# Kernel optimization log

Measured on AMD Instinct MI355X. Metric: run time of the kernel, lower is better.

The kernel has to match this reference:

```python
import jax, jax.numpy as jnp
import numpy as np

# Static hyperparams matching init_kwargs
KSIZE, STRIDE, PAD, DIL = 3, 2, 1, 1


def setup_inputs() -> dict:
    key = jax.random.key(0)
    k1, k2 = jax.random.split(key)
    B, H, W, Cin, Cout = 8, 128, 128, 128, 256
    feats = jax.random.normal(k1, (B * H * W, Cin), dtype=jnp.float32)
    weight = jax.random.normal(k2, (KSIZE * KSIZE, Cin, Cout), dtype=jnp.float32) * 0.05
    alpha_upper = jnp.ones((1,), dtype=jnp.float32)
    # dense grid coords [N, 3] = (batch, y, x), matching a dense image sparse tensor
    bb, yy, xx = np.meshgrid(np.arange(B), np.arange(H), np.arange(W), indexing='ij')
    coords = jnp.asarray(np.stack([bb, yy, xx], -1).reshape(-1, 3), dtype=jnp.int32)
    return {"feats": feats, "weight": weight, "alpha_upper": alpha_upper,
            "coords": coords, "H": H, "W": W, "B": B}


def _coord_ranges(H, W):
    # Faithful translation of WrappedMinkowskiStridedOperation.__init__ + forward
    # coordinate math, specialized to a dense grid (per-batch min=0, max=H-1/W-1).
    kernel_origin = DIL * ((KSIZE - 1) // 2) * (KSIZE % 2)
    dilated = DIL * (KSIZE - 1) + 1
    ks_off = kernel_origin - dilated + 1          # _kernel_start_offset
    ke_off = kernel_origin                        # _kernel_end_offset
    idx_start = kernel_origin - PAD               # _index_start_offset
    ranges = []
    for ext in (H, W):
        idx_end = (ext - 1) + kernel_origin + PAD - dilated + 2
        start = max(idx_start, (0 + ks_off - idx_start) // STRIDE * STRIDE + idx_start)
        end = min(idx_end, ((ext - 1 + ke_off - idx_start) // STRIDE + 1) * STRIDE + idx_start)
        ranges.append(np.arange(start, end, STRIDE))
    offsets = np.arange(KSIZE) * DIL - kernel_origin  # kernel region offsets
    return ranges[0], ranges[1], offsets, idx_start


def reference(feats, weight, alpha_upper, coords, H, W, B):
    Cin = feats.shape[1]
    Cout = weight.shape[-1]
    ys, xs, offs, idx_start = _coord_ranges(H, W)
    OH, OW = len(ys), len(xs)
    oy, ox = jnp.meshgrid(jnp.asarray(ys, jnp.int32), jnp.asarray(xs, jnp.int32), indexing='ij')
    dy, dx = np.meshgrid(offs, offs, indexing='ij')
    dy = jnp.asarray(dy.reshape(-1), jnp.int32)  # [kvol]
    dx = jnp.asarray(dx.reshape(-1), jnp.int32)
    ny = oy[None] + dy[:, None, None]            # [kvol, OH, OW]
    nx = ox[None] + dx[:, None, None]
    valid = (ny >= 0) & (ny < H) & (nx >= 0) & (nx < W)
    lin = jnp.clip(ny, 0, H - 1) * W + jnp.clip(nx, 0, W - 1)  # [kvol, OH, OW]
    feats3 = feats.reshape(B, H * W, Cin)
    gathered = feats3[:, lin]                    # [B, kvol, OH, OW, Cin]
    gathered = jnp.where(valid[None, ..., None], gathered, jnp.zeros((), feats.dtype))
    out = jnp.einsum('bkhwc,kcd->bhwd', gathered, weight)  # [B, OH, OW, Cout]
    out_feats = out.reshape(B * OH * OW, Cout)
    # output coordinates, remapped as in forward (shift by index_start, divide by stride)
    oc = jnp.stack([oy, ox], -1).reshape(-1, 2)  # [OH*OW, 2]
    oc = (oc - jnp.int32(idx_start)) // jnp.int32(STRIDE)
    oc = jnp.tile(oc, (B, 1))
    bcol = jnp.repeat(jnp.arange(B, dtype=jnp.int32), OH * OW)
    out_coords = jnp.concatenate([bcol[:, None], oc], axis=1)
    return out_feats, out_coords, alpha_upper
```

## Files before the change

kernel.cpp:

```cpp
#include <hip/hip_runtime.h>


#define OUT_FEATS_ELEMS (32768 * 256)
#define OUT_COORDS_OFF  OUT_FEATS_ELEMS
#define ALPHA_OFF       (OUT_FEATS_ELEMS + 32768 * 3)

#define BW_BYTES   (18 * 16384)

typedef float v16f __attribute__((ext_vector_type(16)));

__device__ __forceinline__ unsigned pk4fp8(float a, float b, float c, float d) {
    unsigned u = 0;
    u = __builtin_amdgcn_cvt_pk_fp8_f32(a, b, u, false);
    u = __builtin_amdgcn_cvt_pk_fp8_f32(c, d, u, true);
    return u;
}

#define GLOAD_LDS16(SRC, DST)                                                  \
    __builtin_amdgcn_global_load_lds(                                          \
        (const __attribute__((address_space(1))) void*)(SRC),                  \
        (__attribute__((address_space(3))) void*)(DST), 16, 0, 0)

#define WAITBAR_(N) asm volatile("s_waitcnt vmcnt(" #N ")\n\ts_barrier" ::: "memory")
#define WAITBAR(N)  WAITBAR_(N)
#define BAR()       asm volatile("s_barrier" ::: "memory")

__global__ void wprep_kernel(const float* __restrict__ w,
                             const float* __restrict__ alpha,
                             unsigned char* __restrict__ Bw,
                             float* __restrict__ out) {
    int cid = blockIdx.x * 256 + threadIdx.x;
    if (cid < 32768) {
        int b = cid >> 12, iy = (cid >> 6) & 63, ix = cid & 63;
        float* c = out + OUT_COORDS_OFF + (size_t)cid * 3;
        c[0] = (float)b; c[1] = (float)iy; c[2] = (float)ix;
        if (cid == 0) out[ALPHA_OFF] = alpha[0];
    }
    if (cid < 18432) {
        int ch  = cid & 7;
        int row = (cid >> 3) & 127;
        int t   = cid >> 10;
        int nb  = (t >= 9) ? 1 : 0;
        int tap = t - 9 * nb;
        int chp = ch ^ (row & 7);
        int hb  = (row >> 3) & 1;
        int n   = (nb << 7) + row;
        int kb  = (tap << 7) + (chp << 4);
        unsigned u[4];
#pragma unroll
        for (int q = 0; q < 4; ++q) {
            int kq = kb + 4 * (q ^ (hb << 1));
            float f0 = w[(size_t)(kq + 0) * 256 + n];
            float f1 = w[(size_t)(kq + 1) * 256 + n];
            float f2 = w[(size_t)(kq + 2) * 256 + n];
            float f3 = w[(size_t)(kq + 3) * 256 + n];
            u[q] = pk4fp8(f0, f1, f2, f3);
        }
        uint4 r; r.x = u[0]; r.y = u[1]; r.z = u[2]; r.w = u[3];
        *(uint4*)(Bw + (size_t)cid * 16) = r;
    }
}

__global__ void coords_alpha_kernel(float* __restrict__ out, const float* __restrict__ alpha) {
    int i = blockIdx.x * 256 + threadIdx.x;
    int b = i >> 12, iy = (i >> 6) & 63, ix = i & 63;
    float* c = out + OUT_COORDS_OFF + (size_t)i * 3;
    c[0] = (float)b; c[1] = (float)iy; c[2] = (float)ix;
    if (i == 0) out[ALPHA_OFF] = alpha[0];
}

__global__ __launch_bounds__(512, 4) void gemm_conv_kernel(
    const float* __restrict__ feats,
    const unsigned char* __restrict__ Bw,
    float* __restrict__ out)
{
    __shared__ unsigned char Aband[3 * 128 * 128];
    __shared__ unsigned char Bs[256 * 128];

    const int tid  = threadIdx.x;
    const int bid  = blockIdx.x;
    const int my   = ((bid & 7) << 6) + ((bid >> 3) & 63);
    const int m0   = my << 6;
    const int bb   = my >> 6;
    const int iy   = my & 63;

    const int lane = tid & 63, wave = tid >> 6;
    const int wm   = (wave >> 2) << 5;
    const int wn   = (wave & 3) << 6;
    const int l31  = lane & 31;
    const int hh   = lane >> 5;
    const int xorl = l31 & 7;
    const int bhalf = (hh ^ ((l31 >> 3) & 1)) << 3;

    const unsigned char* bsrc0 = Bw + ((size_t)((wave >> 2) * 9) << 14)
                                    + ((size_t)(wave & 3) << 12) + ((size_t)lane << 4);
    auto stageB = [&](int tap) {
        const unsigned char* bs = bsrc0 + ((size_t)tap << 14);
        unsigned char* bdst = Bs + (wave << 12);
#pragma unroll
        for (int q = 0; q < 4; ++q)
            GLOAD_LDS16(bs + (q << 10), bdst + (q << 10));
    };

    stageB(0);

    const int ny0 = (iy << 1) - 1;
    auto issueRow = [&](int r, float4* f) {
        const int ny = ny0 + r;
#pragma unroll
        for (int it = 0; it < 8; ++it) {
            const int idx = (it << 9) + tid;
            const int nx  = idx >> 5;
            const int c4  = (idx & 31) << 2;
            f[it] = *(const float4*)(feats +
                ((((size_t)(bb << 14) + ny * 128 + nx)) << 7) + c4);
        }
    };
    auto writeRow = [&](int r, const float4* f) {
#pragma unroll
        for (int it = 0; it < 8; ++it) {
            const int idx = (it << 9) + tid;
            const int nx  = idx >> 5;
            const int c4  = (idx & 31) << 2;
            const unsigned u = pk4fp8(f[it].x, f[it].y, f[it].z, f[it].w);
            const int key4 = ((nx + 1) >> 1) & 15;
            const int boff = ((r * 128 + nx) << 7)
                + (((c4 >> 4) ^ (key4 & 7)) << 4)
                + (((((c4 >> 3) & 1) ^ (key4 >> 3)) & 1) << 3)
                + (c4 & 7);
            *(unsigned*)(Aband + boff) = u;
        }
    };

    if (iy == 0) {
        for (int z = tid; z < 1024; z += 512) {
            uint4 zz; zz.x = 0u; zz.y = 0u; zz.z = 0u; zz.w = 0u;
            *(uint4*)(Aband + z * 16) = zz;
        }
    }
    {
        float4 fA[8], fB[8];
        const int r0 = (iy == 0) ? 1 : 0;
        issueRow(r0, fA);
        issueRow(r0 + 1, fB);
        writeRow(r0, fA);
        issueRow(2, fA);
        writeRow(r0 + 1, fB);
        if (r0 + 1 != 2) writeRow(2, fA);
        else {  writeRow(2, fA); }
    }
    __syncthreads();

    v16f acc[2];
#pragma unroll
    for (int j = 0; j < 2; j++) acc[j] = (v16f)(0.0f);

    auto computeTap = [&](int dy, int dx) {
        const int r   = dy + 1;
        const int ixv = wm + l31;
        const int nxq = (ixv << 1) + dx;
        const bool pad = (nxq < 0);
        const int nxs = pad ? 0 : nxq;
        const int key4 = ((nxq + 1) >> 1) & 15;
        const int abase = ((r * 128 + nxs) << 7) + ((hh ^ (key4 >> 3)) << 3);
        const int kc = key4 & 7;
#pragma unroll
        for (int seg = 0; seg < 8; ++seg) {
            long long a0 = *(const long long*)(Aband + abase + ((seg ^ kc) << 4));
            if (pad) a0 = 0LL;
            long long b2[2];
#pragma unroll
            for (int j = 0; j < 2; j++)
                b2[j] = *(const long long*)(Bs + ((wn + (j << 5) + l31) << 7)
                                            + ((seg ^ xorl) << 4) + bhalf);
            __builtin_amdgcn_s_setprio(1);
#pragma unroll
            for (int j = 0; j < 2; j++)
                acc[j] = __builtin_amdgcn_mfma_f32_32x32x16_fp8_fp8(a0, b2[j], acc[j], 0, 0, 0);
            __builtin_amdgcn_s_setprio(0);
        }
    };

#pragma unroll
    for (int tap = 0; tap < 9; ++tap) {
        computeTap(tap / 3 - 1, tap % 3 - 1);
        if (tap < 8) {
            BAR();
            stageB(tap + 1);
            WAITBAR(0);
        }
    }

#pragma unroll
    for (int j = 0; j < 2; j++) {
        const int gcol = wn + (j << 5) + l31;
#pragma unroll
        for (int r = 0; r < 16; ++r) {
            const int grow = m0 + wm + (r & 3) + ((r >> 2) << 3) + (hh << 2);
            __builtin_nontemporal_store(acc[j][r], &out[(size_t)grow * 256 + gcol]);
        }
    }
}

__global__ void naive_conv_kernel(const float* __restrict__ feats,
                                  const float* __restrict__ w,
                                  float* __restrict__ out) {
    int m = blockIdx.x;
    int n = threadIdx.x;
    int bb = m >> 12, iy = (m >> 6) & 63, ix = m & 63;
    float acc = 0.f;
    for (int tap = 0; tap < 9; ++tap) {
        int ny = 2 * iy + tap / 3 - 1;
        int nx = 2 * ix + tap % 3 - 1;
        if ((unsigned)ny < 128u && (unsigned)nx < 128u) {
            const float* fr = feats + ((size_t)((bb << 14) + (ny << 7) + nx) << 7);
            const float* wr = w + tap * 32768 + n;
            for (int c = 0; c < 128; ++c) acc += fr[c] * wr[c * 256];
        }
    }
    out[(size_t)m * 256 + n] = acc;
}

extern "C" void kernel_launch(void* const* d_in, const int* in_sizes, int n_in,
                              void* d_out, int out_size, void* d_ws, size_t ws_size,
                              hipStream_t stream) {
    const float* feats  = (const float*)d_in[0];
    const float* weight = (const float*)d_in[1];
    const float* alpha  = (const float*)d_in[2];
    float* out = (float*)d_out;

    const size_t NEED = (size_t)BW_BYTES;
    if (ws_size >= NEED) {
        unsigned char* Bw = (unsigned char*)d_ws;
        wprep_kernel<<<144, 256, 0, stream>>>(weight, alpha, Bw, out);
        gemm_conv_kernel<<<512, 512, 0, stream>>>(feats, Bw, out);
    } else {
        coords_alpha_kernel<<<128, 256, 0, stream>>>(out, alpha);
        naive_conv_kernel<<<32768, 256, 0, stream>>>(feats, weight, out);
    }
}
```

Before: 128.3 us.

## Overlap input-row loading with per-tap MFMA compute in conv GEMM

Instead of loading and converting all three input rows into LDS before any compute, only the first row is staged up front. Rows 1 and 2 are issued as global loads during earlier taps and written to LDS just before they are needed, with lgkmcnt waits added at the barriers that precede their use. This is meant to hide the feature-load latency behind MFMA work. In exchange it cuts the prologue's memory-level parallelism and adds VGPR pressure from keeping row loads in flight across compute.

```diff
diff --git a/kernel.cpp b/kernel.cpp
--- a/kernel.cpp
+++ b/kernel.cpp
@@ -21,9 +21,9 @@
         (const __attribute__((address_space(1))) void*)(SRC),                  \
         (__attribute__((address_space(3))) void*)(DST), 16, 0, 0)
 
-#define WAITBAR_(N) asm volatile("s_waitcnt vmcnt(" #N ")\n\ts_barrier" ::: "memory")
-#define WAITBAR(N)  WAITBAR_(N)
 #define BAR()       asm volatile("s_barrier" ::: "memory")
+#define VMBAR()     asm volatile("s_waitcnt vmcnt(0)\n\ts_barrier" ::: "memory")
+#define VMLGKMBAR() asm volatile("s_waitcnt vmcnt(0) lgkmcnt(0)\n\ts_barrier" ::: "memory")
 
 __global__ void wprep_kernel(const float* __restrict__ w,
                              const float* __restrict__ alpha,
@@ -105,24 +105,25 @@
     stageB(0);
 
     const int ny0 = (iy << 1) - 1;
-    auto issueRow = [&](int r, float4* f) {
+    float4 fR[8];
+    auto issueRow = [&](int r) {
         const int ny = ny0 + r;
 #pragma unroll
         for (int it = 0; it < 8; ++it) {
             const int idx = (it << 9) + tid;
             const int nx  = idx >> 5;
             const int c4  = (idx & 31) << 2;
-            f[it] = *(const float4*)(feats +
+            fR[it] = *(const float4*)(feats +
                 ((((size_t)(bb << 14) + ny * 128 + nx)) << 7) + c4);
         }
     };
-    auto writeRow = [&](int r, const float4* f) {
+    auto writeRow = [&](int r) {
 #pragma unroll
         for (int it = 0; it < 8; ++it) {
             const int idx = (it << 9) + tid;
             const int nx  = idx >> 5;
             const int c4  = (idx & 31) << 2;
-            const unsigned u = pk4fp8(f[it].x, f[it].y, f[it].z, f[it].w);
+            const unsigned u = pk4fp8(fR[it].x, fR[it].y, fR[it].z, fR[it].w);
             const int key4 = ((nx + 1) >> 1) & 15;
             const int boff = ((r * 128 + nx) << 7)
                 + (((c4 >> 4) ^ (key4 & 7)) << 4)
@@ -137,26 +138,17 @@
             uint4 zz; zz.x = 0u; zz.y = 0u; zz.z = 0u; zz.w = 0u;
             *(uint4*)(Aband + z * 16) = zz;
         }
-    }
-    {
-        float4 fA[8], fB[8];
-        const int r0 = (iy == 0) ? 1 : 0;
-        issueRow(r0, fA);
-        issueRow(r0 + 1, fB);
-        writeRow(r0, fA);
-        issueRow(2, fA);
-        writeRow(r0 + 1, fB);
-        if (r0 + 1 != 2) writeRow(2, fA);
-        else {  writeRow(2, fA); }
-    }
-    __syncthreads();
+    } else {
+        issueRow(0);
+        writeRow(0);
+    }
+    VMLGKMBAR();
 
     v16f acc[2];
 #pragma unroll
     for (int j = 0; j < 2; j++) acc[j] = (v16f)(0.0f);
 
-    auto computeTap = [&](int dy, int dx) {
-        const int r   = dy + 1;
+    auto computeTap = [&](int r, int dx) {
         const int ixv = wm + l31;
         const int nxq = (ixv << 1) + dx;
         const bool pad = (nxq < 0);
@@ -181,15 +173,27 @@
         }
     };
 
-#pragma unroll
-    for (int tap = 0; tap < 9; ++tap) {
-        computeTap(tap / 3 - 1, tap % 3 - 1);
-        if (tap < 8) {
-            BAR();
-            stageB(tap + 1);
-            WAITBAR(0);
-        }
-    }
+    issueRow(1);
+    computeTap(0, -1);
+    BAR(); stageB(1); VMBAR();
+    computeTap(0, 0);
+    writeRow(1);
+    issueRow(2);
+    BAR(); stageB(2); VMBAR();
+    computeTap(0, 1);
+    BAR(); stageB(3); VMLGKMBAR();
+    computeTap(1, -1);
+    writeRow(2);
+    BAR(); stageB(4); VMBAR();
+    computeTap(1, 0);
+    BAR(); stageB(5); VMBAR();
+    computeTap(1, 1);
+    BAR(); stageB(6); VMLGKMBAR();
+    computeTap(2, -1);
+    BAR(); stageB(7); VMBAR();
+    computeTap(2, 0);
+    BAR(); stageB(8); VMBAR();
+    computeTap(2, 1);
 
 #pragma unroll
     for (int j = 0; j < 2; j++) {
```

New measurement: 132.1 us. 2.9% more time.
